# Kernel optimization log

Measured on AMD Instinct MI355X. Metric: run time of the kernel, lower is better.

The kernel has to match this reference:

```python
import jax, jax.numpy as jnp
import numpy as np

T, B, D_IN, H = 512, 256, 64, 128


def _normc(key, shape):
    w = jax.random.normal(key, shape, dtype=jnp.float32)
    return w / jnp.sqrt(jnp.sum(w * w, axis=1, keepdims=True))


def setup_inputs() -> dict:
    key = jax.random.key(0)
    ks = jax.random.split(key, 8)
    state = jax.random.normal(ks[0], (T, B, D_IN), dtype=jnp.float32)
    # PyTorch LSTMCell params: weight_ih [4H, in], weight_hh [4H, H], biases [4H]
    s = 1.0 / np.sqrt(H)
    W_ih0 = jax.random.uniform(ks[1], (4 * H, D_IN), minval=-s, maxval=s, dtype=jnp.float32)
    W_hh0 = jax.random.uniform(ks[2], (4 * H, H), minval=-s, maxval=s, dtype=jnp.float32)
    b_ih0 = jnp.zeros((4 * H,), jnp.float32)
    b_hh0 = jnp.zeros((4 * H,), jnp.float32)
    W_ih1 = jax.random.uniform(ks[3], (4 * H, H), minval=-s, maxval=s, dtype=jnp.float32)
    W_hh1 = jax.random.uniform(ks[4], (4 * H, H), minval=-s, maxval=s, dtype=jnp.float32)
    b_ih1 = jnp.zeros((4 * H,), jnp.float32)
    b_hh1 = jnp.zeros((4 * H,), jnp.float32)
    # normc-initialized output head (rows normalized to unit norm, zero bias)
    W_out = _normc(ks[5], (1, H))
    b_out = jnp.zeros((1,), jnp.float32)
    return dict(state=state, W_ih0=W_ih0, W_hh0=W_hh0, b_ih0=b_ih0, b_hh0=b_hh0,
                W_ih1=W_ih1, W_hh1=W_hh1, b_ih1=b_ih1, b_hh1=b_hh1,
                W_out=W_out, b_out=b_out)


def _lstm_cell(x, h, c, W_ih, W_hh, b_ih, b_hh):
    # gates: [B, 4H], chunk order i, f, g, o (PyTorch convention)
    g = x @ W_ih.T + b_ih + h @ W_hh.T + b_hh
    i, f, gg, o = jnp.split(g, 4, axis=-1)
    i = jax.nn.sigmoid(i)
    f = jax.nn.sigmoid(f)
    gg = jnp.tanh(gg)
    o = jax.nn.sigmoid(o)
    c2 = f * c + i * gg
    h2 = o * jnp.tanh(c2)
    return h2, c2


def reference(state, W_ih0, W_hh0, b_ih0, b_hh0, W_ih1, W_hh1, b_ih1, b_hh1, W_out, b_out):
    Bsz = state.shape[1]
    Hd = W_hh0.shape[1]
    z = jnp.zeros((Bsz, Hd), state.dtype)

    def step(carry, x_t):
        h0, c0, h1, c1 = carry
        h0, c0 = _lstm_cell(x_t, h0, c0, W_ih0, W_hh0, b_ih0, b_hh0)
        h1, c1 = _lstm_cell(h0, h1, c1, W_ih1, W_hh1, b_ih1, b_hh1)
        v_t = h1 @ W_out.T + b_out  # [B, 1]
        return (h0, c0, h1, c1), v_t

    _, values = jax.lax.scan(step, (z, z, z, z), state)
    return values  # [T, B, 1]
```

## Files before the change

kernel.cpp:

```cpp
#include <hip/hip_runtime.h>


#define T_STEPS 512
#define BATCH   256
#define DIN     64
#define GROUP   16
#define NGRP    (T_STEPS / GROUP)

typedef _Float16 half8 __attribute__((ext_vector_type(8)));
typedef float    f32x4 __attribute__((ext_vector_type(4)));

#define LOG2E  1.44269504088896f
#define LOG2E2 2.88539008177793f

#define WH_IH0 0
#define WH_HH0 32768
#define WH_IH1 98304
#define WH_HH1 163840
#define WH_X2     229376
#define WH_SLAB2  8617984
#define WB_FLAG2  50790400
#define WS2_TOTAL 50823168
#define WH_SLAB1  229376
#define WB_FLAG1  34013184
#define WS1_TOTAL 34045952
#define WS0XH_TOTAL ((size_t)(WH_X2 + 8388608) * 2)

__global__ void prep_weights(const float* __restrict__ wih0,
                             const float* __restrict__ whh0,
                             const float* __restrict__ wih1,
                             const float* __restrict__ whh1,
                             _Float16* __restrict__ ws) {
    int idx = blockIdx.x * 256 + threadIdx.x;
    float v; int row;
    if (idx < 32768)       { row = idx >> 6;             v = wih0[idx]; }
    else if (idx < 98304)  { row = (idx - 32768) >> 7;   v = whh0[idx - 32768]; }
    else if (idx < 163840) { row = (idx - 98304) >> 7;   v = wih1[idx - 98304]; }
    else                   { row = (idx - 163840) >> 7;  v = whh1[idx - 163840]; }
    float sc = ((row >> 7) == 2) ? LOG2E2 : LOG2E;
    ws[idx] = (_Float16)(v * sc);
}

__global__ void prep_state(const float* __restrict__ s, _Float16* __restrict__ d) {
    int i = (blockIdx.x * 256 + threadIdx.x) * 8;
    f32x4 a = *(const f32x4*)(s + i);
    f32x4 b = *(const f32x4*)(s + i + 4);
    half8 h;
    h[0]=(_Float16)a[0]; h[1]=(_Float16)a[1]; h[2]=(_Float16)a[2]; h[3]=(_Float16)a[3];
    h[4]=(_Float16)b[0]; h[5]=(_Float16)b[1]; h[6]=(_Float16)b[2]; h[7]=(_Float16)b[3];
    *(half8*)(d + i) = h;
}

__device__ __forceinline__ float sig2(float y) {
    return __builtin_amdgcn_rcpf(1.0f + __builtin_amdgcn_exp2f(-y));
}
__device__ __forceinline__ float tanh2(float y2) {
    return 1.0f - 2.0f * __builtin_amdgcn_rcpf(1.0f + __builtin_amdgcn_exp2f(y2));
}
__device__ __forceinline__ float tanh_c(float c) {
    return 1.0f - 2.0f * __builtin_amdgcn_rcpf(1.0f + __builtin_amdgcn_exp2f(c * LOG2E2));
}

#define PIPE_LDS_BYTES ((65536 + 4096 + 128) * 2)

template<bool XH>
__global__ __launch_bounds__(512, 1) void lstm_pipe(
        const float* __restrict__ state32, const _Float16* __restrict__ wsw,
        const float* __restrict__ b_ih0, const float* __restrict__ b_hh0,
        const float* __restrict__ b_ih1, const float* __restrict__ b_hh1,
        const float* __restrict__ w_out, const float* __restrict__ b_out,
        _Float16* __restrict__ slab, int* __restrict__ flags,
        const _Float16* __restrict__ xh, float* __restrict__ out) {
    extern __shared__ _Float16 lds[];
    _Float16* wrec  = lds;
    _Float16* hdb   = lds + 65536;
    _Float16* woutl = lds + 69632;

    const int tid  = threadIdx.x;
    const int w    = tid >> 6;
    const int lane = tid & 63;
    const int col  = lane & 15;
    const int quad = lane >> 4;
    const bool producer = blockIdx.x < 16;
    const int tile = blockIdx.x & 15;
    const int rowbase = tile * 16;
    const int j0 = w * 16 + col;

    const _Float16* wrg = wsw + (producer ? WH_HH0 : WH_HH1);
    #pragma unroll
    for (int it = 0; it < 16; ++it) {
        int flat = (it * 512 + tid) * 8;
        int r = flat >> 7, chunk = (flat >> 3) & 15;
        *(half8*)(wrec + r * 128 + ((chunk ^ (r & 15)) * 8)) = *(const half8*)(wrg + flat);
    }
    {
        half8 z;
        #pragma unroll
        for (int jj = 0; jj < 8; ++jj) z[jj] = (_Float16)0.0f;
        *(half8*)(hdb + tid * 8) = z;
    }
    if (!producer && tid < 128) woutl[tid] = (_Float16)w_out[tid];

    half8 wresf[4][4];
    float bias[4];
    #pragma unroll
    for (int nt = 0; nt < 4; ++nt) {
        int j = nt * 128 + j0;
        float sc = (nt == 2) ? LOG2E2 : LOG2E;
        if (producer) {
            #pragma unroll
            for (int kt = 0; kt < 2; ++kt)
                wresf[nt][kt] = *(const half8*)(wsw + WH_IH0 + j * 64 + kt * 32 + quad * 8);
            bias[nt] = (b_ih0[j] + b_hh0[j]) * sc;
        } else {
            #pragma unroll
            for (int kt = 0; kt < 4; ++kt)
                wresf[nt][kt] = *(const half8*)(wsw + WH_IH1 + j * 128 + kt * 32 + quad * 8);
            bias[nt] = (b_ih1[j] + b_hh1[j]) * sc;
        }
    }
    const float bout = b_out[0];

    int swz[4], hoff[4], w0off[4];
    #pragma unroll
    for (int kt = 0; kt < 4; ++kt) {
        swz[kt]  = ((kt * 4 + quad) ^ col) * 8;
        hoff[kt] = col * 128 + swz[kt];
    }
    #pragma unroll
    for (int i = 0; i < 4; ++i) {
        int row = quad * 4 + i;
        w0off[i] = row * 128 + (((2 * w + (col >> 3)) ^ row) * 8) + (col & 7);
    }
    float cc[4] = {0.f, 0.f, 0.f, 0.f};

    __syncthreads();

    if (producer) {
        const _Float16* xph = xh + (size_t)(rowbase + col) * DIN + quad * 8;
        const float*    xpf = state32 + (size_t)(rowbase + col) * DIN + quad * 8;
        half8 nxh0, nxh1;
        f32x4 nxf0, nxf1, nxf2, nxf3;
        if constexpr (XH) {
            nxh0 = *(const half8*)(xph);
            nxh1 = *(const half8*)(xph + 32);
        } else {
            nxf0 = *(const f32x4*)(xpf);      nxf1 = *(const f32x4*)(xpf + 4);
            nxf2 = *(const f32x4*)(xpf + 32); nxf3 = *(const f32x4*)(xpf + 36);
        }
        _Float16 hh[4];

        #pragma unroll 1
        for (int t = 0; t < T_STEPS; ++t) {
            const int pbo = (t & 1) * 2048, cbo = pbo ^ 2048;
            const int lt = t & (GROUP - 1);
            __syncthreads();

            if (lt == 0) {
                if (t > 0 && tid == 0)
                    __hip_atomic_store(flags + (t / GROUP - 1) * 16 + tile, t / GROUP,
                                       __ATOMIC_RELEASE, __HIP_MEMORY_SCOPE_AGENT);
            } else {
                _Float16* slabP = slab + (size_t)((t - 1) * 16 + tile) * 2048;
                #pragma unroll
                for (int i = 0; i < 4; ++i)
                    slabP[(quad * 4 + i) * 128 + j0] = hh[i];
            }

            half8 ax0, ax1;
            if constexpr (XH) { ax0 = nxh0; ax1 = nxh1; }
            else {
                #pragma unroll
                for (int jj = 0; jj < 4; ++jj) {
                    ax0[jj]   = (_Float16)nxf0[jj]; ax0[jj+4] = (_Float16)nxf1[jj];
                    ax1[jj]   = (_Float16)nxf2[jj]; ax1[jj+4] = (_Float16)nxf3[jj];
                }
            }
            half8 ah[4];
            #pragma unroll
            for (int kt = 0; kt < 4; ++kt)
                ah[kt] = *(const half8*)(hdb + pbo + hoff[kt]);

            f32x4 acc[4];
            #pragma unroll
            for (int nt = 0; nt < 4; ++nt) {
                f32x4 b = {bias[nt], bias[nt], bias[nt], bias[nt]};
                acc[nt] = b;
            }
            #pragma unroll
            for (int kt = 0; kt < 4; ++kt)
                #pragma unroll
                for (int nt = 0; nt < 4; ++nt) {
                    half8 bfr = *(const half8*)(wrec + nt * 16384 + j0 * 128 + swz[kt]);
                    acc[nt] = __builtin_amdgcn_mfma_f32_16x16x32_f16(ah[kt], bfr, acc[nt], 0, 0, 0);
                }
            #pragma unroll
            for (int kt = 0; kt < 2; ++kt) {
                half8 axk = kt ? ax1 : ax0;
                #pragma unroll
                for (int nt = 0; nt < 4; ++nt)
                    acc[nt] = __builtin_amdgcn_mfma_f32_16x16x32_f16(axk, wresf[nt][kt], acc[nt], 0, 0, 0);
            }

            {
                int tn = (t + 1 < T_STEPS) ? t + 1 : t;
                if constexpr (XH) {
                    const _Float16* xq = xph + (size_t)tn * (BATCH * DIN);
                    nxh0 = *(const half8*)(xq);
                    nxh1 = *(const half8*)(xq + 32);
                } else {
                    const float* xq = xpf + (size_t)tn * (BATCH * DIN);
                    nxf0 = *(const f32x4*)(xq);      nxf1 = *(const f32x4*)(xq + 4);
                    nxf2 = *(const f32x4*)(xq + 32); nxf3 = *(const f32x4*)(xq + 36);
                }
            }

            _Float16* slabT = slab + (size_t)(t * 16 + tile) * 2048;
            #pragma unroll
            for (int i = 0; i < 4; ++i) {
                float ig = sig2(acc[0][i]);
                float fg = sig2(acc[1][i]);
                float gg = tanh2(acc[2][i]);
                float og = sig2(acc[3][i]);
                float c  = fg * cc[i] + ig * gg;
                cc[i] = c;
                _Float16 hf = (_Float16)(og * tanh_c(c));
                hdb[cbo + w0off[i]] = hf;
                if (lt == GROUP - 1)
                    slabT[(quad * 4 + i) * 128 + j0] = hf;
                else
                    hh[i] = hf;
            }
        }
        __syncthreads();
        if (tid == 0)
            __hip_atomic_store(flags + (NGRP - 1) * 16 + tile, NGRP,
                               __ATOMIC_RELEASE, __HIP_MEMORY_SCOPE_AGENT);
    } else {
        if (tid == 0) {
            while (__hip_atomic_load(flags + tile, __ATOMIC_ACQUIRE,
                                     __HIP_MEMORY_SCOPE_AGENT) < 1)
                __builtin_amdgcn_s_sleep(1);
        }
        __syncthreads();

        half8 curA[4], nextA[4];
        {
            const _Float16* s0 = slab + (size_t)tile * 2048;
            #pragma unroll
            for (int kt = 0; kt < 4; ++kt)
                curA[kt] = *(const half8*)(s0 + col * 128 + kt * 32 + quad * 8);
        }

        #pragma unroll 1
        for (int t = 0; t < T_STEPS; ++t) {
            const int pbo = (t & 1) * 2048, cbo = pbo ^ 2048;
            const int lt = t & (GROUP - 1);
            __syncthreads();

            half8 a1[4];
            #pragma unroll
            for (int kt = 0; kt < 4; ++kt)
                a1[kt] = *(const half8*)(hdb + pbo + hoff[kt]);

            f32x4 acc[4];
            #pragma unroll
            for (int nt = 0; nt < 4; ++nt) {
                f32x4 b = {bias[nt], bias[nt], bias[nt], bias[nt]};
                acc[nt] = b;
            }
            #pragma unroll
            for (int kt = 0; kt < 4; ++kt)
                #pragma unroll
                for (int nt = 0; nt < 4; ++nt) {
                    half8 bfr = *(const half8*)(wrec + nt * 16384 + j0 * 128 + swz[kt]);
                    acc[nt] = __builtin_amdgcn_mfma_f32_16x16x32_f16(a1[kt], bfr, acc[nt], 0, 0, 0);
                }
            #pragma unroll
            for (int kt = 0; kt < 4; ++kt)
                #pragma unroll
                for (int nt = 0; nt < 4; ++nt)
                    acc[nt] = __builtin_amdgcn_mfma_f32_16x16x32_f16(curA[kt], wresf[nt][kt], acc[nt], 0, 0, 0);

            if (lt == 12 && tid == 0) {
                int g1 = (t >> 4) + 1;
                if (g1 < NGRP) {
                    while (__hip_atomic_load(flags + g1 * 16 + tile, __ATOMIC_ACQUIRE,
                                             __HIP_MEMORY_SCOPE_AGENT) < g1 + 1)
                        __builtin_amdgcn_s_sleep(1);
                }
            }

            {
                int tn = (t + 1 < T_STEPS) ? t + 1 : t;
                const _Float16* sq = slab + (size_t)(tn * 16 + tile) * 2048;
                #pragma unroll
                for (int kt = 0; kt < 4; ++kt)
                    nextA[kt] = *(const half8*)(sq + col * 128 + kt * 32 + quad * 8);
            }

            #pragma unroll
            for (int i = 0; i < 4; ++i) {
                float ig = sig2(acc[0][i]);
                float fg = sig2(acc[1][i]);
                float gg = tanh2(acc[2][i]);
                float og = sig2(acc[3][i]);
                float c  = fg * cc[i] + ig * gg;
                cc[i] = c;
                hdb[cbo + w0off[i]] = (_Float16)(og * tanh_c(c));
            }

            if (w == 7) {
                f32x4 vh = {0.f, 0.f, 0.f, 0.f};
                #pragma unroll
                for (int kt = 0; kt < 4; ++kt) {
                    half8 av = *(const half8*)(hdb + pbo + hoff[kt]);
                    half8 bw = *(const half8*)(woutl + kt * 32 + quad * 8);
                    if (col != 0) {
                        #pragma unroll
                        for (int jj = 0; jj < 8; ++jj) bw[jj] = (_Float16)0.0f;
                    }
                    vh = __builtin_amdgcn_mfma_f32_16x16x32_f16(av, bw, vh, 0, 0, 0);
                }
                if (t > 0 && col == 0) {
                    f32x4 vo = {vh[0] + bout, vh[1] + bout, vh[2] + bout, vh[3] + bout};
                    *(f32x4*)(out + (size_t)(t - 1) * BATCH + rowbase + quad * 4) = vo;
                }
            }

            #pragma unroll
            for (int kt = 0; kt < 4; ++kt) curA[kt] = nextA[kt];
        }
        __syncthreads();
        if (w == 7) {
            const int fbo = (((T_STEPS - 1) & 1) ^ 1) * 2048;
            f32x4 vh = {0.f, 0.f, 0.f, 0.f};
            #pragma unroll
            for (int kt = 0; kt < 4; ++kt) {
                half8 av = *(const half8*)(hdb + fbo + hoff[kt]);
                half8 bw = *(const half8*)(woutl + kt * 32 + quad * 8);
                if (col != 0) {
                    #pragma unroll
                    for (int jj = 0; jj < 8; ++jj) bw[jj] = (_Float16)0.0f;
                }
                vh = __builtin_amdgcn_mfma_f32_16x16x32_f16(av, bw, vh, 0, 0, 0);
            }
            if (col == 0) {
                f32x4 vo = {vh[0] + bout, vh[1] + bout, vh[2] + bout, vh[3] + bout};
                *(f32x4*)(out + (size_t)(T_STEPS - 1) * BATCH + rowbase + quad * 4) = vo;
            }
        }
    }
}

#define MONO_LDS_BYTES ((73728 + 128) * 2)

template<bool XH>
__global__ __launch_bounds__(512, 2) void lstm_mono(
        const float* __restrict__ state32, const _Float16* __restrict__ wsw,
        const float* __restrict__ b_ih0, const float* __restrict__ b_hh0,
        const float* __restrict__ b_ih1, const float* __restrict__ b_hh1,
        const float* __restrict__ w_out, const float* __restrict__ b_out,
        float* __restrict__ out) {
    extern __shared__ _Float16 lds[];
    _Float16* whh1  = lds;
    _Float16* h0b   = lds + 65536;
    _Float16* h1b   = lds + 69632;
    _Float16* woutl = lds + 73728;

    const int tid  = threadIdx.x;
    const int w    = tid >> 6;
    const int lane = tid & 63;
    const int col  = lane & 15;
    const int quad = lane >> 4;
    const int rowbase = blockIdx.x * 16;
    const int j0 = w * 16 + col;

    const _Float16* whh1g = wsw + WH_HH1;
    #pragma unroll
    for (int it = 0; it < 16; ++it) {
        int flat = (it * 512 + tid) * 8;
        int r = flat >> 7, chunk = (flat >> 3) & 15;
        *(half8*)(whh1 + r * 128 + ((chunk ^ (r & 15)) * 8)) = *(const half8*)(whh1g + flat);
    }
    {
        half8 z;
        #pragma unroll
        for (int jj = 0; jj < 8; ++jj) z[jj] = (_Float16)0.0f;
        for (int i = tid * 8; i < 8192; i += 4096) *(half8*)(h0b + i) = z;
    }
    if (tid < 128) woutl[tid] = (_Float16)w_out[tid];

    half8 whh0f[4][4], wih1f[4][4];
    float bias0[4], bias1[4];
    #pragma unroll
    for (int nt = 0; nt < 4; ++nt) {
        int j = nt * 128 + j0;
        float sc = (nt == 2) ? LOG2E2 : LOG2E;
        #pragma unroll
        for (int kt = 0; kt < 4; ++kt) {
            whh0f[nt][kt] = *(const half8*)(wsw + WH_HH0 + j * 128 + kt * 32 + quad * 8);
            wih1f[nt][kt] = *(const half8*)(wsw + WH_IH1 + j * 128 + kt * 32 + quad * 8);
        }
        bias0[nt] = (b_ih0[j] + b_hh0[j]) * sc;
        bias1[nt] = (b_ih1[j] + b_hh1[j]) * sc;
    }
    const float bout = b_out[0];

    int swz[4], hoff[4], w0off[4];
    #pragma unroll
    for (int kt = 0; kt < 4; ++kt) {
        swz[kt]  = ((kt * 4 + quad) ^ col) * 8;
        hoff[kt] = col * 128 + swz[kt];
    }
    #pragma unroll
    for (int i = 0; i < 4; ++i) {
        int row = quad * 4 + i;
        w0off[i] = row * 128 + (((2 * w + (col >> 3)) ^ row) * 8) + (col & 7);
    }
    float c0[4] = {0.f,0.f,0.f,0.f}, c1[4] = {0.f,0.f,0.f,0.f};

    const _Float16* xph = wsw + WH_X2 + (size_t)(rowbase + col) * DIN + quad * 8;
    const float*    xpf = state32 + (size_t)(rowbase + col) * DIN + quad * 8;
    half8 nxh0, nxh1;
    f32x4 nxf0, nxf1, nxf2, nxf3;
    if constexpr (XH) {
        nxh0 = *(const half8*)(xph); nxh1 = *(const half8*)(xph + 32);
    } else {
        nxf0 = *(const f32x4*)(xpf);      nxf1 = *(const f32x4*)(xpf + 4);
        nxf2 = *(const f32x4*)(xpf + 32); nxf3 = *(const f32x4*)(xpf + 36);
    }
    __syncthreads();
    const _Float16* wih0g = wsw + WH_IH0;

    #pragma unroll 1
    for (int t = 0; t < T_STEPS; ++t) {
        const int pbo = (t & 1) * 2048, cbo = pbo ^ 2048;
        half8 ax0, ax1;
        if constexpr (XH) { ax0 = nxh0; ax1 = nxh1; }
        else {
            #pragma unroll
            for (int jj = 0; jj < 4; ++jj) {
                ax0[jj]   = (_Float16)nxf0[jj]; ax0[jj+4] = (_Float16)nxf1[jj];
                ax1[jj]   = (_Float16)nxf2[jj]; ax1[jj+4] = (_Float16)nxf3[jj];
            }
        }
        half8 wif[4][2];
        #pragma unroll
        for (int nt = 0; nt < 4; ++nt)
            #pragma unroll
            for (int kt = 0; kt < 2; ++kt)
                wif[nt][kt] = *(const half8*)(wih0g + (nt * 128 + j0) * 64 + kt * 32 + quad * 8);
        half8 ah[4];
        #pragma unroll
        for (int kt = 0; kt < 4; ++kt)
            ah[kt] = *(const half8*)(h0b + pbo + hoff[kt]);

        f32x4 acc[4];
        #pragma unroll
        for (int nt = 0; nt < 4; ++nt) {
            f32x4 b = {bias0[nt], bias0[nt], bias0[nt], bias0[nt]};
            acc[nt] = b;
        }
        #pragma unroll
        for (int kt = 0; kt < 4; ++kt)
            #pragma unroll
            for (int nt = 0; nt < 4; ++nt)
                acc[nt] = __builtin_amdgcn_mfma_f32_16x16x32_f16(ah[kt], whh0f[nt][kt], acc[nt], 0, 0, 0);
        #pragma unroll
        for (int kt = 0; kt < 2; ++kt) {
            half8 axk = kt ? ax1 : ax0;
            #pragma unroll
            for (int nt = 0; nt < 4; ++nt)
                acc[nt] = __builtin_amdgcn_mfma_f32_16x16x32_f16(axk, wif[nt][kt], acc[nt], 0, 0, 0);
        }
        {
            int tn = (t + 1 < T_STEPS) ? t + 1 : t;
            if constexpr (XH) {
                const _Float16* xq = xph + (size_t)tn * (BATCH * DIN);
                nxh0 = *(const half8*)(xq); nxh1 = *(const half8*)(xq + 32);
            } else {
                const float* xq = xpf + (size_t)tn * (BATCH * DIN);
                nxf0 = *(const f32x4*)(xq);      nxf1 = *(const f32x4*)(xq + 4);
                nxf2 = *(const f32x4*)(xq + 32); nxf3 = *(const f32x4*)(xq + 36);
            }
        }
        #pragma unroll
        for (int i = 0; i < 4; ++i) {
            float ig = sig2(acc[0][i]);
            float fg = sig2(acc[1][i]);
            float gg = tanh2(acc[2][i]);
            float og = sig2(acc[3][i]);
            float c  = fg * c0[i] + ig * gg;
            c0[i] = c;
            h0b[cbo + w0off[i]] = (_Float16)(og * tanh_c(c));
        }
        __syncthreads();

        #pragma unroll
        for (int nt = 0; nt < 4; ++nt) {
            f32x4 b = {bias1[nt], bias1[nt], bias1[nt], bias1[nt]};
            acc[nt] = b;
        }
        #pragma unroll
        for (int kt = 0; kt < 4; ++kt) {
            half8 a0 = *(const half8*)(h0b + cbo + hoff[kt]);
            half8 a1 = *(const half8*)(h1b + pbo + hoff[kt]);
            #pragma unroll
            for (int nt = 0; nt < 4; ++nt)
                acc[nt] = __builtin_amdgcn_mfma_f32_16x16x32_f16(a0, wih1f[nt][kt], acc[nt], 0, 0, 0);
            #pragma unroll
            for (int nt = 0; nt < 4; ++nt) {
                half8 bfr = *(const half8*)(whh1 + nt * 16384 + j0 * 128 + swz[kt]);
                acc[nt] = __builtin_amdgcn_mfma_f32_16x16x32_f16(a1, bfr, acc[nt], 0, 0, 0);
            }
        }
        #pragma unroll
        for (int i = 0; i < 4; ++i) {
            float ig = sig2(acc[0][i]);
            float fg = sig2(acc[1][i]);
            float gg = tanh2(acc[2][i]);
            float og = sig2(acc[3][i]);
            float c  = fg * c1[i] + ig * gg;
            c1[i] = c;
            h1b[cbo + w0off[i]] = (_Float16)(og * tanh_c(c));
        }
        if (w == 7) {
            f32x4 vh = {0.f, 0.f, 0.f, 0.f};
            #pragma unroll
            for (int kt = 0; kt < 4; ++kt) {
                half8 a1 = *(const half8*)(h1b + pbo + hoff[kt]);
                half8 bw = *(const half8*)(woutl + kt * 32 + quad * 8);
                if (col != 0) {
                    #pragma unroll
                    for (int jj = 0; jj < 8; ++jj) bw[jj] = (_Float16)0.0f;
                }
                vh = __builtin_amdgcn_mfma_f32_16x16x32_f16(a1, bw, vh, 0, 0, 0);
            }
            if (t > 0 && col == 0) {
                f32x4 vo = {vh[0] + bout, vh[1] + bout, vh[2] + bout, vh[3] + bout};
                *(f32x4*)(out + (size_t)(t - 1) * BATCH + rowbase + quad * 4) = vo;
            }
        }
    }
    __syncthreads();
    if (w == 7) {
        const int fbo = (((T_STEPS - 1) & 1) ^ 1) * 2048;
        f32x4 vh = {0.f, 0.f, 0.f, 0.f};
        #pragma unroll
        for (int kt = 0; kt < 4; ++kt) {
            half8 a1 = *(const half8*)(h1b + fbo + hoff[kt]);
            half8 bw = *(const half8*)(woutl + kt * 32 + quad * 8);
            if (col != 0) {
                #pragma unroll
                for (int jj = 0; jj < 8; ++jj) bw[jj] = (_Float16)0.0f;
            }
            vh = __builtin_amdgcn_mfma_f32_16x16x32_f16(a1, bw, vh, 0, 0, 0);
        }
        if (col == 0) {
            f32x4 vo = {vh[0] + bout, vh[1] + bout, vh[2] + bout, vh[3] + bout};
            *(f32x4*)(out + (size_t)(T_STEPS - 1) * BATCH + rowbase + quad * 4) = vo;
        }
    }
}

extern "C" void kernel_launch(void* const* d_in, const int* in_sizes, int n_in,
                              void* d_out, int out_size, void* d_ws, size_t ws_size,
                              hipStream_t stream) {
    const float* state = (const float*)d_in[0];
    const float* wih0  = (const float*)d_in[1];
    const float* whh0  = (const float*)d_in[2];
    const float* bih0  = (const float*)d_in[3];
    const float* bhh0  = (const float*)d_in[4];
    const float* wih1  = (const float*)d_in[5];
    const float* whh1  = (const float*)d_in[6];
    const float* bih1  = (const float*)d_in[7];
    const float* bhh1  = (const float*)d_in[8];
    const float* wout  = (const float*)d_in[9];
    const float* bout  = (const float*)d_in[10];
    _Float16* wsh = (_Float16*)d_ws;
    float* outp = (float*)d_out;

    prep_weights<<<896, 256, 0, stream>>>(wih0, whh0, wih1, whh1, wsh);

    if (ws_size >= WS2_TOTAL) {
        prep_state<<<4096, 256, 0, stream>>>(state, wsh + WH_X2);
        lstm_pipe<true><<<32, 512, PIPE_LDS_BYTES, stream>>>(
            state, wsh, bih0, bhh0, bih1, bhh1, wout, bout,
            wsh + WH_SLAB2, (int*)((char*)d_ws + WB_FLAG2), wsh + WH_X2, outp);
    } else if (ws_size >= WS1_TOTAL) {
        lstm_pipe<false><<<32, 512, PIPE_LDS_BYTES, stream>>>(
            state, wsh, bih0, bhh0, bih1, bhh1, wout, bout,
            wsh + WH_SLAB1, (int*)((char*)d_ws + WB_FLAG1), nullptr, outp);
    } else if (ws_size >= WS0XH_TOTAL) {
        prep_state<<<4096, 256, 0, stream>>>(state, wsh + WH_X2);
        lstm_mono<true><<<16, 512, MONO_LDS_BYTES, stream>>>(
            state, wsh, bih0, bhh0, bih1, bhh1, wout, bout, outp);
    } else {
        lstm_mono<false><<<16, 512, MONO_LDS_BYTES, stream>>>(
            state, wsh, bih0, bhh0, bih1, bhh1, wout, bout, outp);
    }
}
```

Baseline: 713.9 us.

## Offload output head to dedicated workgroups fed via global h1 slab

Adds a third pipeline stage: 16 extra workgroups compute the value head from layer-1 hidden states that consumer blocks write to a global slab, signalled with per-group flags. This removes the per-step wave-7 head MFMA and output store from the serial recurrence critical path of the layer-1 blocks. In exchange the consumers do extra scattered fp16 global stores each step plus flag releases, and the path needs a larger workspace; if the workspace is too small it falls back to the old path.

```diff
diff --git a/kernel.cpp b/kernel.cpp
--- a/kernel.cpp
+++ b/kernel.cpp
@@ -19,6 +19,9 @@
 #define WH_HH1 163840
 #define WH_X2     229376
 #define WH_SLAB2  8617984
+#define WH_SLB2H  25395200
+#define WB_FLAG3  84344832
+#define WS3_TOTAL 84377600
 #define WB_FLAG2  50790400
 #define WS2_TOTAL 50823168
 #define WH_SLAB1  229376
@@ -63,13 +66,14 @@
 
 #define PIPE_LDS_BYTES ((65536 + 4096 + 128) * 2)
 
-template<bool XH>
+template<bool XH, bool HO>
 __global__ __launch_bounds__(512, 1) void lstm_pipe(
         const float* __restrict__ state32, const _Float16* __restrict__ wsw,
         const float* __restrict__ b_ih0, const float* __restrict__ b_hh0,
         const float* __restrict__ b_ih1, const float* __restrict__ b_hh1,
         const float* __restrict__ w_out, const float* __restrict__ b_out,
-        _Float16* __restrict__ slab, int* __restrict__ flags,
+        _Float16* __restrict__ slab, _Float16* __restrict__ slab2,
+        int* __restrict__ flags,
         const _Float16* __restrict__ xh, float* __restrict__ out) {
     extern __shared__ _Float16 lds[];
     _Float16* wrec  = lds;
@@ -82,9 +86,58 @@
     const int col  = lane & 15;
     const int quad = lane >> 4;
     const bool producer = blockIdx.x < 16;
+    const bool headwg   = HO && blockIdx.x >= 32;
     const int tile = blockIdx.x & 15;
     const int rowbase = tile * 16;
     const int j0 = w * 16 + col;
+    int* hflags = flags + 4096;
+    const float bout = b_out[0];
+
+    if (headwg) {
+        half8 bwf[4];
+        #pragma unroll
+        for (int kt = 0; kt < 4; ++kt) {
+            half8 bw;
+            if (col == 0) {
+                f32x4 wa = *(const f32x4*)(w_out + kt * 32 + quad * 8);
+                f32x4 wb = *(const f32x4*)(w_out + kt * 32 + quad * 8 + 4);
+                #pragma unroll
+                for (int jj = 0; jj < 4; ++jj) {
+                    bw[jj]     = (_Float16)wa[jj];
+                    bw[jj + 4] = (_Float16)wb[jj];
+                }
+            } else {
+                #pragma unroll
+                for (int jj = 0; jj < 8; ++jj) bw[jj] = (_Float16)0.0f;
+            }
+            bwf[kt] = bw;
+        }
+        #pragma unroll 1
+        for (int g = 0; g < NGRP; ++g) {
+            if (tid == 0) {
+                while (__hip_atomic_load(hflags + g * 16 + tile, __ATOMIC_ACQUIRE,
+                                         __HIP_MEMORY_SCOPE_AGENT) < g + 1)
+                    __builtin_amdgcn_s_sleep(2);
+            }
+            __syncthreads();
+            #pragma unroll
+            for (int s = 0; s < 2; ++s) {
+                int t = g * GROUP + w + s * 8;
+                const _Float16* sq = slab2 + (size_t)(t * 16 + tile) * 2048;
+                f32x4 vh = {0.f, 0.f, 0.f, 0.f};
+                #pragma unroll
+                for (int kt = 0; kt < 4; ++kt) {
+                    half8 av = *(const half8*)(sq + col * 128 + kt * 32 + quad * 8);
+                    vh = __builtin_amdgcn_mfma_f32_16x16x32_f16(av, bwf[kt], vh, 0, 0, 0);
+                }
+                if (col == 0) {
+                    f32x4 vo = {vh[0] + bout, vh[1] + bout, vh[2] + bout, vh[3] + bout};
+                    *(f32x4*)(out + (size_t)t * BATCH + rowbase + quad * 4) = vo;
+                }
+            }
+        }
+        return;
+    }
 
     const _Float16* wrg = wsw + (producer ? WH_HH0 : WH_HH1);
     #pragma unroll
@@ -99,7 +152,7 @@
         for (int jj = 0; jj < 8; ++jj) z[jj] = (_Float16)0.0f;
         *(half8*)(hdb + tid * 8) = z;
     }
-    if (!producer && tid < 128) woutl[tid] = (_Float16)w_out[tid];
+    if (!HO && !producer && tid < 128) woutl[tid] = (_Float16)w_out[tid];
 
     half8 wresf[4][4];
     float bias[4];
@@ -119,7 +172,6 @@
             bias[nt] = (b_ih1[j] + b_hh1[j]) * sc;
         }
     }
-    const float bout = b_out[0];
 
     int swz[4], hoff[4], w0off[4];
     #pragma unroll
@@ -251,12 +303,26 @@
             for (int kt = 0; kt < 4; ++kt)
                 curA[kt] = *(const half8*)(s0 + col * 128 + kt * 32 + quad * 8);
         }
+        _Float16 hh1[4];
 
         #pragma unroll 1
         for (int t = 0; t < T_STEPS; ++t) {
             const int pbo = (t & 1) * 2048, cbo = pbo ^ 2048;
             const int lt = t & (GROUP - 1);
             __syncthreads();
+
+            if constexpr (HO) {
+                if (lt == 0) {
+                    if (t > 0 && tid == 0)
+                        __hip_atomic_store(hflags + (t / GROUP - 1) * 16 + tile, t / GROUP,
+                                           __ATOMIC_RELEASE, __HIP_MEMORY_SCOPE_AGENT);
+                } else {
+                    _Float16* s2P = slab2 + (size_t)((t - 1) * 16 + tile) * 2048;
+                    #pragma unroll
+                    for (int i = 0; i < 4; ++i)
+                        s2P[(quad * 4 + i) * 128 + j0] = hh1[i];
+                }
+            }
 
             half8 a1[4];
             #pragma unroll
@@ -299,6 +365,7 @@
                     nextA[kt] = *(const half8*)(sq + col * 128 + kt * 32 + quad * 8);
             }
 
+            _Float16* s2T = slab2 + (size_t)(t * 16 + tile) * 2048;
             #pragma unroll
             for (int i = 0; i < 4; ++i) {
                 float ig = sig2(acc[0][i]);
@@ -307,14 +374,51 @@
                 float og = sig2(acc[3][i]);
                 float c  = fg * cc[i] + ig * gg;
                 cc[i] = c;
-                hdb[cbo + w0off[i]] = (_Float16)(og * tanh_c(c));
-            }
-
+                _Float16 hf = (_Float16)(og * tanh_c(c));
+                hdb[cbo + w0off[i]] = hf;
+                if constexpr (HO) {
+                    if (lt == GROUP - 1)
+                        s2T[(quad * 4 + i) * 128 + j0] = hf;
+                    else
+                        hh1[i] = hf;
+                }
+            }
+
+            if constexpr (!HO) {
+                if (w == 7) {
+                    f32x4 vh = {0.f, 0.f, 0.f, 0.f};
+                    #pragma unroll
+                    for (int kt = 0; kt < 4; ++kt) {
+                        half8 av = *(const half8*)(hdb + pbo + hoff[kt]);
+                        half8 bw = *(const half8*)(woutl + kt * 32 + quad * 8);
+                        if (col != 0) {
+                            #pragma unroll
+                            for (int jj = 0; jj < 8; ++jj) bw[jj] = (_Float16)0.0f;
+                        }
+                        vh = __builtin_amdgcn_mfma_f32_16x16x32_f16(av, bw, vh, 0, 0, 0);
+                    }
+                    if (t > 0 && col == 0) {
+                        f32x4 vo = {vh[0] + bout, vh[1] + bout, vh[2] + bout, vh[3] + bout};
+                        *(f32x4*)(out + (size_t)(t - 1) * BATCH + rowbase + quad * 4) = vo;
+                    }
+                }
+            }
+
+            #pragma unroll
+            for (int kt = 0; kt < 4; ++kt) curA[kt] = nextA[kt];
+        }
+        __syncthreads();
+        if constexpr (HO) {
+            if (tid == 0)
+                __hip_atomic_store(hflags + (NGRP - 1) * 16 + tile, NGRP,
+                                   __ATOMIC_RELEASE, __HIP_MEMORY_SCOPE_AGENT);
+        } else {
             if (w == 7) {
+                const int fbo = (((T_STEPS - 1) & 1) ^ 1) * 2048;
                 f32x4 vh = {0.f, 0.f, 0.f, 0.f};
                 #pragma unroll
                 for (int kt = 0; kt < 4; ++kt) {
-                    half8 av = *(const half8*)(hdb + pbo + hoff[kt]);
+                    half8 av = *(const half8*)(hdb + fbo + hoff[kt]);
                     half8 bw = *(const half8*)(woutl + kt * 32 + quad * 8);
                     if (col != 0) {
                         #pragma unroll
@@ -322,32 +426,10 @@
                     }
                     vh = __builtin_amdgcn_mfma_f32_16x16x32_f16(av, bw, vh, 0, 0, 0);
                 }
-                if (t > 0 && col == 0) {
+                if (col == 0) {
                     f32x4 vo = {vh[0] + bout, vh[1] + bout, vh[2] + bout, vh[3] + bout};
-                    *(f32x4*)(out + (size_t)(t - 1) * BATCH + rowbase + quad * 4) = vo;
-                }
-            }
-
-            #pragma unroll
-            for (int kt = 0; kt < 4; ++kt) curA[kt] = nextA[kt];
-        }
-        __syncthreads();
-        if (w == 7) {
-            const int fbo = (((T_STEPS - 1) & 1) ^ 1) * 2048;
-            f32x4 vh = {0.f, 0.f, 0.f, 0.f};
-            #pragma unroll
-            for (int kt = 0; kt < 4; ++kt) {
-                half8 av = *(const half8*)(hdb + fbo + hoff[kt]);
-                half8 bw = *(const half8*)(woutl + kt * 32 + quad * 8);
-                if (col != 0) {
-                    #pragma unroll
-                    for (int jj = 0; jj < 8; ++jj) bw[jj] = (_Float16)0.0f;
-                }
-                vh = __builtin_amdgcn_mfma_f32_16x16x32_f16(av, bw, vh, 0, 0, 0);
-            }
-            if (col == 0) {
-                f32x4 vo = {vh[0] + bout, vh[1] + bout, vh[2] + bout, vh[3] + bout};
-                *(f32x4*)(out + (size_t)(T_STEPS - 1) * BATCH + rowbase + quad * 4) = vo;
+                    *(f32x4*)(out + (size_t)(T_STEPS - 1) * BATCH + rowbase + quad * 4) = vo;
+                }
             }
         }
     }
@@ -583,15 +665,23 @@
 
     prep_weights<<<896, 256, 0, stream>>>(wih0, whh0, wih1, whh1, wsh);
 
-    if (ws_size >= WS2_TOTAL) {
+    if (ws_size >= WS3_TOTAL) {
         prep_state<<<4096, 256, 0, stream>>>(state, wsh + WH_X2);
-        lstm_pipe<true><<<32, 512, PIPE_LDS_BYTES, stream>>>(
+        lstm_pipe<true, true><<<48, 512, PIPE_LDS_BYTES, stream>>>(
             state, wsh, bih0, bhh0, bih1, bhh1, wout, bout,
-            wsh + WH_SLAB2, (int*)((char*)d_ws + WB_FLAG2), wsh + WH_X2, outp);
+            wsh + WH_SLAB2, wsh + WH_SLB2H, (int*)((char*)d_ws + WB_FLAG3),
+            wsh + WH_X2, outp);
+    } else if (ws_size >= WS2_TOTAL) {
+        prep_state<<<4096, 256, 0, stream>>>(state, wsh + WH_X2);
+        lstm_pipe<true, false><<<32, 512, PIPE_LDS_BYTES, stream>>>(
+            state, wsh, bih0, bhh0, bih1, bhh1, wout, bout,
+            wsh + WH_SLAB2, nullptr, (int*)((char*)d_ws + WB_FLAG2),
+            wsh + WH_X2, outp);
     } else if (ws_size >= WS1_TOTAL) {
-        lstm_pipe<false><<<32, 512, PIPE_LDS_BYTES, stream>>>(
+        lstm_pipe<false, false><<<32, 512, PIPE_LDS_BYTES, stream>>>(
             state, wsh, bih0, bhh0, bih1, bhh1, wout, bout,
-            wsh + WH_SLAB1, (int*)((char*)d_ws + WB_FLAG1), nullptr, outp);
+            wsh + WH_SLAB1, nullptr, (int*)((char*)d_ws + WB_FLAG1),
+            nullptr, outp);
     } else if (ws_size >= WS0XH_TOTAL) {
         prep_state<<<4096, 256, 0, stream>>>(state, wsh + WH_X2);
         lstm_mono<true><<<16, 512, MONO_LDS_BYTES, stream>>>(
```

New measurement: 798.7 us. 11.9% more time.

## Software-pipeline input projections one step ahead in both LSTM layers

Applied to the files above, without the earlier changes.

Both the producer (layer 0) and consumer (layer 1) loops now compute the input-side MFMA product (x or h0 times W_ih, plus bias) for step t+1 during step t. The recurrent part of step t then starts from that precomputed accumulator. Operand prefetch moves from one step ahead to two, and the loops are unrolled by 2. The aim is to take the input matmuls off the serial h-dependent critical path so they overlap with the gate activations, at the cost of more live registers and a deeper prefetch that must stay consistent with the flag waits.

```diff
diff --git a/kernel.cpp b/kernel.cpp
--- a/kernel.cpp
+++ b/kernel.cpp
@@ -139,18 +139,48 @@
     if (producer) {
         const _Float16* xph = xh + (size_t)(rowbase + col) * DIN + quad * 8;
         const float*    xpf = state32 + (size_t)(rowbase + col) * DIN + quad * 8;
-        half8 nxh0, nxh1;
-        f32x4 nxf0, nxf1, nxf2, nxf3;
-        if constexpr (XH) {
-            nxh0 = *(const half8*)(xph);
-            nxh1 = *(const half8*)(xph + 32);
-        } else {
-            nxf0 = *(const f32x4*)(xpf);      nxf1 = *(const f32x4*)(xpf + 4);
-            nxf2 = *(const f32x4*)(xpf + 32); nxf3 = *(const f32x4*)(xpf + 36);
+
+        half8 bx0, bx1;
+        f32x4 bf0, bf1, bf2, bf3;
+        f32x4 accI[4];
+        {
+            half8 a0, a1v;
+            if constexpr (XH) {
+                a0  = *(const half8*)(xph);
+                a1v = *(const half8*)(xph + 32);
+            } else {
+                f32x4 t0 = *(const f32x4*)(xpf),      t1 = *(const f32x4*)(xpf + 4);
+                f32x4 t2 = *(const f32x4*)(xpf + 32), t3 = *(const f32x4*)(xpf + 36);
+                #pragma unroll
+                for (int jj = 0; jj < 4; ++jj) {
+                    a0[jj]  = (_Float16)t0[jj]; a0[jj+4]  = (_Float16)t1[jj];
+                    a1v[jj] = (_Float16)t2[jj]; a1v[jj+4] = (_Float16)t3[jj];
+                }
+            }
+            #pragma unroll
+            for (int nt = 0; nt < 4; ++nt) {
+                f32x4 b = {bias[nt], bias[nt], bias[nt], bias[nt]};
+                accI[nt] = b;
+            }
+            #pragma unroll
+            for (int nt = 0; nt < 4; ++nt)
+                accI[nt] = __builtin_amdgcn_mfma_f32_16x16x32_f16(a0, wresf[nt][0], accI[nt], 0, 0, 0);
+            #pragma unroll
+            for (int nt = 0; nt < 4; ++nt)
+                accI[nt] = __builtin_amdgcn_mfma_f32_16x16x32_f16(a1v, wresf[nt][1], accI[nt], 0, 0, 0);
+            if constexpr (XH) {
+                bx0 = *(const half8*)(xph + BATCH * DIN);
+                bx1 = *(const half8*)(xph + BATCH * DIN + 32);
+            } else {
+                bf0 = *(const f32x4*)(xpf + BATCH * DIN);
+                bf1 = *(const f32x4*)(xpf + BATCH * DIN + 4);
+                bf2 = *(const f32x4*)(xpf + BATCH * DIN + 32);
+                bf3 = *(const f32x4*)(xpf + BATCH * DIN + 36);
+            }
         }
         _Float16 hh[4];
 
-        #pragma unroll 1
+        #pragma unroll 2
         for (int t = 0; t < T_STEPS; ++t) {
             const int pbo = (t & 1) * 2048, cbo = pbo ^ 2048;
             const int lt = t & (GROUP - 1);
@@ -167,61 +197,65 @@
                     slabP[(quad * 4 + i) * 128 + j0] = hh[i];
             }
 
-            half8 ax0, ax1;
-            if constexpr (XH) { ax0 = nxh0; ax1 = nxh1; }
-            else {
-                #pragma unroll
-                for (int jj = 0; jj < 4; ++jj) {
-                    ax0[jj]   = (_Float16)nxf0[jj]; ax0[jj+4] = (_Float16)nxf1[jj];
-                    ax1[jj]   = (_Float16)nxf2[jj]; ax1[jj+4] = (_Float16)nxf3[jj];
-                }
-            }
             half8 ah[4];
             #pragma unroll
             for (int kt = 0; kt < 4; ++kt)
                 ah[kt] = *(const half8*)(hdb + pbo + hoff[kt]);
 
-            f32x4 acc[4];
-            #pragma unroll
-            for (int nt = 0; nt < 4; ++nt) {
-                f32x4 b = {bias[nt], bias[nt], bias[nt], bias[nt]};
-                acc[nt] = b;
-            }
             #pragma unroll
             for (int kt = 0; kt < 4; ++kt)
                 #pragma unroll
                 for (int nt = 0; nt < 4; ++nt) {
                     half8 bfr = *(const half8*)(wrec + nt * 16384 + j0 * 128 + swz[kt]);
-                    acc[nt] = __builtin_amdgcn_mfma_f32_16x16x32_f16(ah[kt], bfr, acc[nt], 0, 0, 0);
-                }
-            #pragma unroll
-            for (int kt = 0; kt < 2; ++kt) {
-                half8 axk = kt ? ax1 : ax0;
+                    accI[nt] = __builtin_amdgcn_mfma_f32_16x16x32_f16(ah[kt], bfr, accI[nt], 0, 0, 0);
+                }
+
+            half8 fx0, fx1;
+            f32x4 ff0, ff1, ff2, ff3;
+            {
+                int tn2 = (t + 2 < T_STEPS) ? t + 2 : T_STEPS - 1;
+                if constexpr (XH) {
+                    const _Float16* xq = xph + (size_t)tn2 * (BATCH * DIN);
+                    fx0 = *(const half8*)(xq);
+                    fx1 = *(const half8*)(xq + 32);
+                } else {
+                    const float* xq = xpf + (size_t)tn2 * (BATCH * DIN);
+                    ff0 = *(const f32x4*)(xq);      ff1 = *(const f32x4*)(xq + 4);
+                    ff2 = *(const f32x4*)(xq + 32); ff3 = *(const f32x4*)(xq + 36);
+                }
+            }
+
+            f32x4 accN[4];
+            {
+                half8 c0, c1;
+                if constexpr (XH) { c0 = bx0; c1 = bx1; }
+                else {
+                    #pragma unroll
+                    for (int jj = 0; jj < 4; ++jj) {
+                        c0[jj] = (_Float16)bf0[jj]; c0[jj+4] = (_Float16)bf1[jj];
+                        c1[jj] = (_Float16)bf2[jj]; c1[jj+4] = (_Float16)bf3[jj];
+                    }
+                }
+                #pragma unroll
+                for (int nt = 0; nt < 4; ++nt) {
+                    f32x4 b = {bias[nt], bias[nt], bias[nt], bias[nt]};
+                    accN[nt] = b;
+                }
                 #pragma unroll
                 for (int nt = 0; nt < 4; ++nt)
-                    acc[nt] = __builtin_amdgcn_mfma_f32_16x16x32_f16(axk, wresf[nt][kt], acc[nt], 0, 0, 0);
-            }
-
-            {
-                int tn = (t + 1 < T_STEPS) ? t + 1 : t;
-                if constexpr (XH) {
-                    const _Float16* xq = xph + (size_t)tn * (BATCH * DIN);
-                    nxh0 = *(const half8*)(xq);
-                    nxh1 = *(const half8*)(xq + 32);
-                } else {
-                    const float* xq = xpf + (size_t)tn * (BATCH * DIN);
-                    nxf0 = *(const f32x4*)(xq);      nxf1 = *(const f32x4*)(xq + 4);
-                    nxf2 = *(const f32x4*)(xq + 32); nxf3 = *(const f32x4*)(xq + 36);
-                }
+                    accN[nt] = __builtin_amdgcn_mfma_f32_16x16x32_f16(c0, wresf[nt][0], accN[nt], 0, 0, 0);
+                #pragma unroll
+                for (int nt = 0; nt < 4; ++nt)
+                    accN[nt] = __builtin_amdgcn_mfma_f32_16x16x32_f16(c1, wresf[nt][1], accN[nt], 0, 0, 0);
             }
 
             _Float16* slabT = slab + (size_t)(t * 16 + tile) * 2048;
             #pragma unroll
             for (int i = 0; i < 4; ++i) {
-                float ig = sig2(acc[0][i]);
-                float fg = sig2(acc[1][i]);
-                float gg = tanh2(acc[2][i]);
-                float og = sig2(acc[3][i]);
+                float ig = sig2(accI[0][i]);
+                float fg = sig2(accI[1][i]);
+                float gg = tanh2(accI[2][i]);
+                float og = sig2(accI[3][i]);
                 float c  = fg * cc[i] + ig * gg;
                 cc[i] = c;
                 _Float16 hf = (_Float16)(og * tanh_c(c));
@@ -231,6 +265,11 @@
                 else
                     hh[i] = hf;
             }
+
+            #pragma unroll
+            for (int nt = 0; nt < 4; ++nt) accI[nt] = accN[nt];
+            if constexpr (XH) { bx0 = fx0; bx1 = fx1; }
+            else { bf0 = ff0; bf1 = ff1; bf2 = ff2; bf3 = ff3; }
         }
         __syncthreads();
         if (tid == 0)
@@ -244,15 +283,31 @@
         }
         __syncthreads();
 
-        half8 curA[4], nextA[4];
+        half8 uA[4];
+        f32x4 accI[4];
         {
             const _Float16* s0 = slab + (size_t)tile * 2048;
-            #pragma unroll
-            for (int kt = 0; kt < 4; ++kt)
-                curA[kt] = *(const half8*)(s0 + col * 128 + kt * 32 + quad * 8);
-        }
-
-        #pragma unroll 1
+            half8 cA[4];
+            #pragma unroll
+            for (int kt = 0; kt < 4; ++kt)
+                cA[kt] = *(const half8*)(s0 + col * 128 + kt * 32 + quad * 8);
+            #pragma unroll
+            for (int nt = 0; nt < 4; ++nt) {
+                f32x4 b = {bias[nt], bias[nt], bias[nt], bias[nt]};
+                accI[nt] = b;
+            }
+            #pragma unroll
+            for (int kt = 0; kt < 4; ++kt)
+                #pragma unroll
+                for (int nt = 0; nt < 4; ++nt)
+                    accI[nt] = __builtin_amdgcn_mfma_f32_16x16x32_f16(cA[kt], wresf[nt][kt], accI[nt], 0, 0, 0);
+            const _Float16* s1 = slab + (size_t)(16 + tile) * 2048;
+            #pragma unroll
+            for (int kt = 0; kt < 4; ++kt)
+                uA[kt] = *(const half8*)(s1 + col * 128 + kt * 32 + quad * 8);
+        }
+
+        #pragma unroll 2
         for (int t = 0; t < T_STEPS; ++t) {
             const int pbo = (t & 1) * 2048, cbo = pbo ^ 2048;
             const int lt = t & (GROUP - 1);
@@ -263,24 +318,13 @@
             for (int kt = 0; kt < 4; ++kt)
                 a1[kt] = *(const half8*)(hdb + pbo + hoff[kt]);
 
-            f32x4 acc[4];
-            #pragma unroll
-            for (int nt = 0; nt < 4; ++nt) {
-                f32x4 b = {bias[nt], bias[nt], bias[nt], bias[nt]};
-                acc[nt] = b;
-            }
             #pragma unroll
             for (int kt = 0; kt < 4; ++kt)
                 #pragma unroll
                 for (int nt = 0; nt < 4; ++nt) {
                     half8 bfr = *(const half8*)(wrec + nt * 16384 + j0 * 128 + swz[kt]);
-                    acc[nt] = __builtin_amdgcn_mfma_f32_16x16x32_f16(a1[kt], bfr, acc[nt], 0, 0, 0);
-                }
-            #pragma unroll
-            for (int kt = 0; kt < 4; ++kt)
-                #pragma unroll
-                for (int nt = 0; nt < 4; ++nt)
-                    acc[nt] = __builtin_amdgcn_mfma_f32_16x16x32_f16(curA[kt], wresf[nt][kt], acc[nt], 0, 0, 0);
+                    accI[nt] = __builtin_amdgcn_mfma_f32_16x16x32_f16(a1[kt], bfr, accI[nt], 0, 0, 0);
+                }
 
             if (lt == 12 && tid == 0) {
                 int g1 = (t >> 4) + 1;
@@ -291,20 +335,33 @@
                 }
             }
 
+            half8 fA[4];
             {
-                int tn = (t + 1 < T_STEPS) ? t + 1 : t;
-                const _Float16* sq = slab + (size_t)(tn * 16 + tile) * 2048;
+                int tn2 = (t + 2 < T_STEPS) ? t + 2 : T_STEPS - 1;
+                const _Float16* sq = slab + (size_t)(tn2 * 16 + tile) * 2048;
                 #pragma unroll
                 for (int kt = 0; kt < 4; ++kt)
-                    nextA[kt] = *(const half8*)(sq + col * 128 + kt * 32 + quad * 8);
-            }
+                    fA[kt] = *(const half8*)(sq + col * 128 + kt * 32 + quad * 8);
+            }
+
+            f32x4 accN[4];
+            #pragma unroll
+            for (int nt = 0; nt < 4; ++nt) {
+                f32x4 b = {bias[nt], bias[nt], bias[nt], bias[nt]};
+                accN[nt] = b;
+            }
+            #pragma unroll
+            for (int kt = 0; kt < 4; ++kt)
+                #pragma unroll
+                for (int nt = 0; nt < 4; ++nt)
+                    accN[nt] = __builtin_amdgcn_mfma_f32_16x16x32_f16(uA[kt], wresf[nt][kt], accN[nt], 0, 0, 0);
 
             #pragma unroll
             for (int i = 0; i < 4; ++i) {
-                float ig = sig2(acc[0][i]);
-                float fg = sig2(acc[1][i]);
-                float gg = tanh2(acc[2][i]);
-                float og = sig2(acc[3][i]);
+                float ig = sig2(accI[0][i]);
+                float fg = sig2(accI[1][i]);
+                float gg = tanh2(accI[2][i]);
+                float og = sig2(accI[3][i]);
                 float c  = fg * cc[i] + ig * gg;
                 cc[i] = c;
                 hdb[cbo + w0off[i]] = (_Float16)(og * tanh_c(c));
@@ -329,7 +386,9 @@
             }
 
             #pragma unroll
-            for (int kt = 0; kt < 4; ++kt) curA[kt] = nextA[kt];
+            for (int nt = 0; nt < 4; ++nt) accI[nt] = accN[nt];
+            #pragma unroll
+            for (int kt = 0; kt < 4; ++kt) uA[kt] = fA[kt];
         }
         __syncthreads();
         if (w == 7) {
```

Result: faster. 691.1 us (-3.2%).
